# Kernel tuning notes

Measured on AMD Instinct MI355X. Metric: run time of the kernel, lower is better.

The kernel has to match this reference:

```python
import jax, jax.numpy as jnp
import numpy as np

B, N, G, D, H = 32, 512, 512, 512, 16
KD = D // H            # key_dim = embedding_dim // head_num
CLIP = 10.0            # tanh logit clipping


def _heads(x):
    # [B, C, D] -> [B, H, C, KD]
    b, c, _ = x.shape
    return x.reshape(b, c, H, KD).transpose(0, 2, 1, 3)


def setup_inputs() -> dict:
    key = jax.random.key(0)
    ks = jax.random.split(key, 9)
    s = 0.02
    return {
        "encoded_nodes": jax.random.normal(ks[0], (B, N, D), jnp.float32),
        "encoded_last": jax.random.normal(ks[1], (B, G, D), jnp.float32),
        "group_ninf_mask": jnp.zeros((B, G, N), jnp.float32),
        "Wq_graph": jax.random.normal(ks[2], (D, D), jnp.float32) * s,
        "Wq_first": jax.random.normal(ks[3], (D, D), jnp.float32) * s,
        "Wq_last": jax.random.normal(ks[4], (D, D), jnp.float32) * s,
        "Wk": jax.random.normal(ks[5], (D, D), jnp.float32) * s,
        "Wv": jax.random.normal(ks[6], (D, D), jnp.float32) * s,
        "Wcomb": jax.random.normal(ks[7], (D, D), jnp.float32) * s,
        "bcomb": jnp.zeros((D,), jnp.float32),
    }


def reference(encoded_nodes, encoded_last, group_ninf_mask,
              Wq_graph, Wq_first, Wq_last, Wk, Wv, Wcomb, bcomb):
    # reset(): graph embedding = mean over nodes, keys/values from encoded_nodes
    graph = encoded_nodes.mean(axis=1, keepdims=True)            # [B,1,D]
    q = (_heads(graph @ Wq_graph.T)                              # [B,H,1,KD] broadcast
         + _heads(encoded_last @ Wq_first.T)                     # q_first (first call)
         + _heads(encoded_last @ Wq_last.T))                     # [B,H,G,KD]
    k = _heads(encoded_nodes @ Wk.T)                             # [B,H,N,KD]
    v = _heads(encoded_nodes @ Wv.T)                             # [B,H,N,KD]

    # stage 1: masked multi-head attention
    score = jnp.einsum('bhgk,bhnk->bhgn', q, k) / float(np.sqrt(KD))
    score = score + group_ninf_mask[:, None, :, :]
    w = jax.nn.softmax(score, axis=-1)
    out = jnp.einsum('bhgn,bhnk->bhgk', w, v)
    out = out.transpose(0, 2, 1, 3).reshape(-1, G, D)            # [B,G,D]
    mh = out @ Wcomb.T + bcomb

    # stage 2: single-head score -> scale -> tanh clip -> mask -> softmax
    s2 = jnp.einsum('bgd,bnd->bgn', mh, encoded_nodes) / float(np.sqrt(D))
    s2 = CLIP * jnp.tanh(s2) + group_ninf_mask
    return jax.nn.softmax(s2, axis=-1)
```

## Files before the change

kernel.cpp:

```cpp
#include <hip/hip_runtime.h>
#include <hip/hip_bf16.h>
#include <stdint.h>
#include <math.h>

#define B_  32
#define N_  512
#define G_  512
#define D_  512
#define H_  16
#define KD_ 32

using bf16x8 = __attribute__((ext_vector_type(8))) short;
using f32x4  = __attribute__((ext_vector_type(4))) float;
typedef unsigned short u16;

__device__ __forceinline__ u16 f2b(float x) {
  union { __hip_bfloat16 h; u16 u; } c;
  c.h = __float2bfloat16(x);
  return c.u;
}
__device__ __forceinline__ float b2f(u16 u) {
  union { float f; unsigned int i; } c;
  c.i = ((unsigned int)u) << 16;
  return c.f;
}

__device__ __forceinline__ void async16(void* lds, const void* g) {
  __builtin_amdgcn_global_load_lds(
      (const __attribute__((address_space(1))) unsigned int*)(uintptr_t)g,
      (__attribute__((address_space(3))) unsigned int*)(uintptr_t)lds,
      16, 0, 0);
}

__global__ __launch_bounds__(512) void mean_split_kernel(
    const float* __restrict__ enc, u16* __restrict__ hi, u16* __restrict__ lo,
    float* __restrict__ partial)
{
  const int b  = blockIdx.x;
  const int nc = blockIdx.y;
  const int d  = threadIdx.x;
  const size_t base = ((size_t)b * N_ + (size_t)nc * 64) * D_ + d;
  float psum = 0.f;
  for (int i = 0; i < 64; ++i) {
    float v = enc[base + (size_t)i * D_];
    psum += v;
    u16 h = f2b(v);
    hi[base + (size_t)i * D_] = h;
    lo[base + (size_t)i * D_] = f2b(v - b2f(h));
  }
  partial[((size_t)b * 8 + nc) * D_ + d] = psum;
}

__global__ __launch_bounds__(512) void mean_final_kernel(
    const float* __restrict__ partial, float* __restrict__ graph)
{
  const int b = blockIdx.x, d = threadIdx.x;
  float s = 0.f;
  for (int c = 0; c < 8; ++c) s += partial[((size_t)b * 8 + c) * D_ + d];
  graph[b * D_ + d] = s * (1.0f / N_);
}

__global__ void split4_kernel(const float* __restrict__ in,
                              u16* __restrict__ hi, u16* __restrict__ lo, int n4)
{
  int i = blockIdx.x * blockDim.x + threadIdx.x;
  if (i < n4) {
    float4 v = ((const float4*)in)[i];
    ushort4 h, l;
    h.x = f2b(v.x); l.x = f2b(v.x - b2f(h.x));
    h.y = f2b(v.y); l.y = f2b(v.y - b2f(h.y));
    h.z = f2b(v.z); l.z = f2b(v.z - b2f(h.z));
    h.w = f2b(v.w); l.w = f2b(v.w - b2f(h.w));
    ((ushort4*)hi)[i] = h;
    ((ushort4*)lo)[i] = l;
  }
}

__global__ void wsum_split_kernel(const float* __restrict__ a, const float* __restrict__ b,
                                  u16* __restrict__ hi, u16* __restrict__ lo, int n4)
{
  int i = blockIdx.x * blockDim.x + threadIdx.x;
  if (i < n4) {
    float4 va = ((const float4*)a)[i];
    float4 vb = ((const float4*)b)[i];
    float x0 = va.x + vb.x, x1 = va.y + vb.y, x2 = va.z + vb.z, x3 = va.w + vb.w;
    ushort4 h, l;
    h.x = f2b(x0); l.x = f2b(x0 - b2f(h.x));
    h.y = f2b(x1); l.y = f2b(x1 - b2f(h.y));
    h.z = f2b(x2); l.z = f2b(x2 - b2f(h.z));
    h.w = f2b(x3); l.w = f2b(x3 - b2f(h.w));
    ((ushort4*)hi)[i] = h;
    ((ushort4*)lo)[i] = l;
  }
}

__global__ __launch_bounds__(256) void qg_kernel(
    const float* __restrict__ graph, const float* __restrict__ Wq,
    float* __restrict__ qg)
{
  const int b  = blockIdx.y;
  const int dd = blockIdx.x * 256 + threadIdx.x;
  const float* g = graph + b * D_;
  const float* w = Wq + (size_t)dd * D_;
  float s = 0.f;
  for (int k = 0; k < D_; ++k) s += g[k] * w[k];
  qg[b * D_ + dd] = s;
}

__global__ __launch_bounds__(256) void rowmax_kernel(
    const float* __restrict__ mask, float* __restrict__ rmx)
{
  const int row  = blockIdx.x * 4 + (threadIdx.x >> 6);
  const int lane = threadIdx.x & 63;
  const float* r = mask + (size_t)row * N_;
  float4 a  = *(const float4*)&r[lane * 8];
  float4 b4 = *(const float4*)&r[lane * 8 + 4];
  float m = fmaxf(fmaxf(fmaxf(a.x, a.y), fmaxf(a.z, a.w)),
                  fmaxf(fmaxf(b4.x, b4.y), fmaxf(b4.z, b4.w)));
#pragma unroll
  for (int w = 1; w < 64; w <<= 1) m = fmaxf(m, __shfl_xor(m, w));
  if (lane == 0) rmx[row] = m;
}

__global__ __launch_bounds__(64) void kmax_kernel(
    const u16* __restrict__ khi, float* __restrict__ kmx)
{
  const int b = blockIdx.x >> 4, h = blockIdx.x & 15;
  const int lane = threadIdx.x;
  float mx = 0.f;
  for (int i = 0; i < 8; ++i) {
    const int n = i * 64 + lane;
    const unsigned int* p =
        (const unsigned int*)&khi[((size_t)b * 512 + n) * 512 + h * 32];
    float s = 0.f;
#pragma unroll
    for (int w = 0; w < 16; ++w) {
      unsigned int u = p[w];
      float f0 = __uint_as_float(u << 16);
      float f1 = __uint_as_float(u & 0xffff0000u);
      s = fmaf(f0, f0, s);
      s = fmaf(f1, f1, s);
    }
    mx = fmaxf(mx, s);
  }
#pragma unroll
  for (int w = 1; w < 64; w <<= 1) mx = fmaxf(mx, __shfl_xor(mx, w));
  if (lane == 0) kmx[blockIdx.x] = sqrtf(mx) * 1.01f;
}

template<int OUTMODE, int BIASMODE>
__global__ __launch_bounds__(256) void gemm_split_kernel(
    const u16* __restrict__ Ahi, const u16* __restrict__ Alo,
    const u16* __restrict__ Bhi, const u16* __restrict__ Blo,
    void* __restrict__ Chi, void* __restrict__ Clo,
    void* __restrict__ Dhi, void* __restrict__ Dlo,
    const float* __restrict__ bias,
    int M, int N, int K)
{
  __shared__ __align__(16) u16 AhS[4096], AlS[4096], BhS[4096], BlS[4096];

  const int brow = blockIdx.y * 128;
  const int bcol = blockIdx.x * 128;
  const int tid  = threadIdx.x;
  const int wid  = tid >> 6;
  const int lane = tid & 63;
  const int wr = wid >> 1, wc = wid & 1;

  f32x4 acc[4][4] = {};

  const int c0   = wid * 2;
  const int srow = lane >> 2;
  const int skk  = (lane & 3) * 8;

  const size_t g0 = (size_t)(brow + c0 * 16      + srow) * K + skk;
  const size_t g1 = (size_t)(brow + c0 * 16 + 16 + srow) * K + skk;
  const size_t h0 = (size_t)(bcol + c0 * 16      + srow) * K + skk;
  const size_t h1 = (size_t)(bcol + c0 * 16 + 16 + srow) * K + skk;
  u16* lA0 = &AhS[c0 * 512]; u16* lA1 = &AhS[c0 * 512 + 512];
  u16* la0 = &AlS[c0 * 512]; u16* la1 = &AlS[c0 * 512 + 512];
  u16* lB0 = &BhS[c0 * 512]; u16* lB1 = &BhS[c0 * 512 + 512];
  u16* lb0 = &BlS[c0 * 512]; u16* lb1 = &BlS[c0 * 512 + 512];

  const int aoff = (wr * 64 + (lane & 15)) * 32 + (lane >> 4) * 8;
  const int boff = (wc * 64 + (lane & 15)) * 32 + (lane >> 4) * 8;

  for (int k0 = 0; k0 < K; k0 += 32) {
    async16(lA0, Ahi + g0 + k0);
    async16(lA1, Ahi + g1 + k0);
    async16(la0, Alo + g0 + k0);
    async16(la1, Alo + g1 + k0);
    async16(lB0, Bhi + h0 + k0);
    async16(lB1, Bhi + h1 + k0);
    async16(lb0, Blo + h0 + k0);
    async16(lb1, Blo + h1 + k0);
    __syncthreads();

    bf16x8 ah[4], al[4], bh[4], bl[4];
#pragma unroll
    for (int m = 0; m < 4; ++m) {
      ah[m] = *(const bf16x8*)&AhS[aoff + m * 512];
      al[m] = *(const bf16x8*)&AlS[aoff + m * 512];
    }
#pragma unroll
    for (int n = 0; n < 4; ++n) {
      bh[n] = *(const bf16x8*)&BhS[boff + n * 512];
      bl[n] = *(const bf16x8*)&BlS[boff + n * 512];
    }
#pragma unroll
    for (int m = 0; m < 4; ++m)
#pragma unroll
      for (int n = 0; n < 4; ++n) {
        f32x4 t = acc[m][n];
        t = __builtin_amdgcn_mfma_f32_16x16x32_bf16(al[m], bh[n], t, 0, 0, 0);
        t = __builtin_amdgcn_mfma_f32_16x16x32_bf16(ah[m], bl[n], t, 0, 0, 0);
        t = __builtin_amdgcn_mfma_f32_16x16x32_bf16(ah[m], bh[n], t, 0, 0, 0);
        acc[m][n] = t;
      }
    __syncthreads();
  }

  const int r0 = brow + wr * 64 + (lane >> 4) * 4;
  const int cbase = bcol + wc * 64 + (lane & 15);
#pragma unroll
  for (int m = 0; m < 4; ++m) {
#pragma unroll
    for (int n = 0; n < 4; ++n) {
      const int c = cbase + n * 16;
#pragma unroll
      for (int j = 0; j < 4; ++j) {
        const int r = r0 + m * 16 + j;
        float v = acc[m][n][j];
        if (BIASMODE == 1) v += bias[(r >> 9) * 512 + c];
        if (BIASMODE == 2) v += bias[c];
        u16 hv = f2b(v);
        u16 lv = f2b(v - b2f(hv));
        if (OUTMODE == 1) {
          ((u16*)Chi)[(size_t)r * N + c] = hv;
          ((u16*)Clo)[(size_t)r * N + c] = lv;
        } else {
          if (c < 512) {
            ((u16*)Chi)[(size_t)r * 512 + c] = hv;
            ((u16*)Clo)[(size_t)r * 512 + c] = lv;
          } else {
            const int bb = r >> 9, nn = r & 511, hh = (c >> 5) & 15, dd = c & 31;
            const size_t idx = (((size_t)bb * 16 + hh) * 32 + dd) * 512 + nn;
            ((u16*)Dhi)[idx] = hv;
            ((u16*)Dlo)[idx] = lv;
          }
        }
      }
    }
  }
}

__global__ __launch_bounds__(256) void attn_mfma5_kernel(
    u16* __restrict__ Qhi, u16* __restrict__ Qlo,
    const u16* __restrict__ Khi, const u16* __restrict__ Klo,
    const u16* __restrict__ VThi, const u16* __restrict__ VTlo,
    const float* __restrict__ mask,
    const float* __restrict__ rowmaxb,
    const float* __restrict__ kmaxb)
{
  __shared__ __align__(16) u16 Ph[4][32][56], Pl[4][32][56];

  const int tid = threadIdx.x, wid = tid >> 6, lane = tid & 63;
  const int id   = blockIdx.x;
  const int h    = id & 15;
  const int gblk = (id >> 4) & 3;
  const int b    = id >> 6;
  const int g0   = gblk * 128 + wid * 32;
  const int colq = lane & 15, rowg = lane >> 4;

  const size_t qb = ((size_t)b * G_ + g0) * D_ + h * KD_;
  const size_t kb = ((size_t)b * N_) * D_ + h * KD_;
  const size_t vb = (((size_t)b * H_ + h) * KD_) * (size_t)N_;
  const float* Mb = mask + ((size_t)b * G_ + g0) * N_;

  bf16x8 qh[2], ql[2];
  qh[0] = *(const bf16x8*)&Qhi[qb + (size_t)colq * D_ + rowg * 8];
  ql[0] = *(const bf16x8*)&Qlo[qb + (size_t)colq * D_ + rowg * 8];
  qh[1] = *(const bf16x8*)&Qhi[qb + (size_t)(16 + colq) * D_ + rowg * 8];
  ql[1] = *(const bf16x8*)&Qlo[qb + (size_t)(16 + colq) * D_ + rowg * 8];

  const float scale = 0.17677669529663687f;
  const f32x4 zf = {0.f, 0.f, 0.f, 0.f};
  const bf16x8 ones = {0x3F80, 0x3F80, 0x3F80, 0x3F80, 0x3F80, 0x3F80, 0x3F80, 0x3F80};

  const float km = kmaxb[b * 16 + h];
  float nq2[2];
#pragma unroll
  for (int rf = 0; rf < 2; ++rf) {
    float s = 0.f;
    const unsigned int* qw = (const unsigned int*)&qh[rf];
#pragma unroll
    for (int w = 0; w < 4; ++w) {
      unsigned int u = qw[w];
      float f0 = __uint_as_float(u << 16);
      float f1 = __uint_as_float(u & 0xffff0000u);
      s = fmaf(f0, f0, s);
      s = fmaf(f1, f1, s);
    }
    s += __shfl_xor(s, 16);
    s += __shfl_xor(s, 32);
    nq2[rf] = s;
  }
  float mrow[2][4];
#pragma unroll
  for (int rf = 0; rf < 2; ++rf)
#pragma unroll
    for (int j = 0; j < 4; ++j) {
      const int r16 = rowg * 4 + j;
      float nq = sqrtf(__shfl(nq2[rf], r16)) * 1.01f;
      mrow[rf][j] = scale * nq * km + rowmaxb[(size_t)b * G_ + g0 + rf * 16 + r16];
    }

  f32x4 o[2][2] = {};
  f32x4 os[2] = {};

  for (int n0 = 0; n0 < N_; n0 += 32) {
    bf16x8 kh0 = *(const bf16x8*)&Khi[kb + (size_t)(n0 + colq) * D_ + rowg * 8];
    bf16x8 kl0 = *(const bf16x8*)&Klo[kb + (size_t)(n0 + colq) * D_ + rowg * 8];
    bf16x8 kh1 = *(const bf16x8*)&Khi[kb + (size_t)(n0 + 16 + colq) * D_ + rowg * 8];
    bf16x8 kl1 = *(const bf16x8*)&Klo[kb + (size_t)(n0 + 16 + colq) * D_ + rowg * 8];
    bf16x8 vh0 = *(const bf16x8*)&VThi[vb + (size_t)colq * N_ + n0 + rowg * 8];
    bf16x8 vl0 = *(const bf16x8*)&VTlo[vb + (size_t)colq * N_ + n0 + rowg * 8];
    bf16x8 vh1 = *(const bf16x8*)&VThi[vb + (size_t)(16 + colq) * N_ + n0 + rowg * 8];
    bf16x8 vl1 = *(const bf16x8*)&VTlo[vb + (size_t)(16 + colq) * N_ + n0 + rowg * 8];

#pragma unroll
    for (int rf = 0; rf < 2; ++rf) {
      __builtin_amdgcn_s_setprio(1);
      f32x4 t0 = __builtin_amdgcn_mfma_f32_16x16x32_bf16(ql[rf], kh0, zf, 0, 0, 0);
      t0 = __builtin_amdgcn_mfma_f32_16x16x32_bf16(qh[rf], kl0, t0, 0, 0, 0);
      t0 = __builtin_amdgcn_mfma_f32_16x16x32_bf16(qh[rf], kh0, t0, 0, 0, 0);
      f32x4 t1 = __builtin_amdgcn_mfma_f32_16x16x32_bf16(ql[rf], kh1, zf, 0, 0, 0);
      t1 = __builtin_amdgcn_mfma_f32_16x16x32_bf16(qh[rf], kl1, t1, 0, 0, 0);
      t1 = __builtin_amdgcn_mfma_f32_16x16x32_bf16(qh[rf], kh1, t1, 0, 0, 0);
      __builtin_amdgcn_s_setprio(0);
#pragma unroll
      for (int j = 0; j < 4; ++j) {
        const int gg = rf * 16 + rowg * 4 + j;
        float m0 = Mb[(size_t)gg * N_ + n0 + colq];
        float m1 = Mb[(size_t)gg * N_ + n0 + 16 + colq];
        float p0 = __expf(fmaf(t0[j], scale, m0 - mrow[rf][j]));
        float p1 = __expf(fmaf(t1[j], scale, m1 - mrow[rf][j]));
        unsigned int uh, ul;
        asm("v_cvt_pk_bf16_f32 %0, %1, %2" : "=v"(uh) : "v"(p0), "v"(p1));
        float h0f = __uint_as_float(uh << 16);
        float h1f = __uint_as_float(uh & 0xffff0000u);
        float l0 = p0 - h0f, l1 = p1 - h1f;
        asm("v_cvt_pk_bf16_f32 %0, %1, %2" : "=v"(ul) : "v"(l0), "v"(l1));
        Ph[wid][gg][colq]      = (u16)uh;
        Ph[wid][gg][16 + colq] = (u16)(uh >> 16);
        Pl[wid][gg][colq]      = (u16)ul;
        Pl[wid][gg][16 + colq] = (u16)(ul >> 16);
      }
    }
    asm volatile("s_waitcnt lgkmcnt(0)" ::: "memory");

    bf16x8 ph0 = *(const bf16x8*)&Ph[wid][colq][rowg * 8];
    bf16x8 pl0 = *(const bf16x8*)&Pl[wid][colq][rowg * 8];
    bf16x8 ph1 = *(const bf16x8*)&Ph[wid][16 + colq][rowg * 8];
    bf16x8 pl1 = *(const bf16x8*)&Pl[wid][16 + colq][rowg * 8];

    __builtin_amdgcn_s_setprio(1);
    o[0][0] = __builtin_amdgcn_mfma_f32_16x16x32_bf16(pl0, vh0, o[0][0], 0, 0, 0);
    o[0][0] = __builtin_amdgcn_mfma_f32_16x16x32_bf16(ph0, vl0, o[0][0], 0, 0, 0);
    o[0][0] = __builtin_amdgcn_mfma_f32_16x16x32_bf16(ph0, vh0, o[0][0], 0, 0, 0);
    o[0][1] = __builtin_amdgcn_mfma_f32_16x16x32_bf16(pl0, vh1, o[0][1], 0, 0, 0);
    o[0][1] = __builtin_amdgcn_mfma_f32_16x16x32_bf16(ph0, vl1, o[0][1], 0, 0, 0);
    o[0][1] = __builtin_amdgcn_mfma_f32_16x16x32_bf16(ph0, vh1, o[0][1], 0, 0, 0);
    o[1][0] = __builtin_amdgcn_mfma_f32_16x16x32_bf16(pl1, vh0, o[1][0], 0, 0, 0);
    o[1][0] = __builtin_amdgcn_mfma_f32_16x16x32_bf16(ph1, vl0, o[1][0], 0, 0, 0);
    o[1][0] = __builtin_amdgcn_mfma_f32_16x16x32_bf16(ph1, vh0, o[1][0], 0, 0, 0);
    o[1][1] = __builtin_amdgcn_mfma_f32_16x16x32_bf16(pl1, vh1, o[1][1], 0, 0, 0);
    o[1][1] = __builtin_amdgcn_mfma_f32_16x16x32_bf16(ph1, vl1, o[1][1], 0, 0, 0);
    o[1][1] = __builtin_amdgcn_mfma_f32_16x16x32_bf16(ph1, vh1, o[1][1], 0, 0, 0);
    os[0] = __builtin_amdgcn_mfma_f32_16x16x32_bf16(ph0, ones, os[0], 0, 0, 0);
    os[0] = __builtin_amdgcn_mfma_f32_16x16x32_bf16(pl0, ones, os[0], 0, 0, 0);
    os[1] = __builtin_amdgcn_mfma_f32_16x16x32_bf16(ph1, ones, os[1], 0, 0, 0);
    os[1] = __builtin_amdgcn_mfma_f32_16x16x32_bf16(pl1, ones, os[1], 0, 0, 0);
    __builtin_amdgcn_s_setprio(0);
  }

#pragma unroll
  for (int rf = 0; rf < 2; ++rf)
#pragma unroll
    for (int j = 0; j < 4; ++j) {
      const float inv = 1.f / os[rf][j];
      const int gg = rf * 16 + rowg * 4 + j;
      float v0 = o[rf][0][j] * inv;
      float v1 = o[rf][1][j] * inv;
      u16 h0 = f2b(v0), h1 = f2b(v1);
      Qhi[qb + (size_t)gg * D_ + colq]      = h0;
      Qlo[qb + (size_t)gg * D_ + colq]      = f2b(v0 - b2f(h0));
      Qhi[qb + (size_t)gg * D_ + 16 + colq] = h1;
      Qlo[qb + (size_t)gg * D_ + 16 + colq] = f2b(v1 - b2f(h1));
    }
}

__global__ __launch_bounds__(256) void s2fused_kernel(
    const u16* __restrict__ Ahi, const u16* __restrict__ Alo,
    const u16* __restrict__ Bhi, const u16* __restrict__ Blo,
    const float* __restrict__ mask, float* __restrict__ out)
{
  __shared__ __align__(16) u16 AhS[2048], AlS[2048];
  __shared__ __align__(16) u16 BhS[16384], BlS[16384];

  const int z    = blockIdx.y;
  const int brow = blockIdx.x * 64;
  const int tid  = threadIdx.x;
  const int wid  = tid >> 6;
  const int lane = tid & 63;
  const int colq = lane & 15, rowg = lane >> 4;

  const u16* Az_hi = Ahi + (size_t)z * 262144;
  const u16* Az_lo = Alo + (size_t)z * 262144;
  const u16* Bz_hi = Bhi + (size_t)z * 262144;
  const u16* Bz_lo = Blo + (size_t)z * 262144;

  f32x4 acc[32] = {};

  const int srow = lane >> 2;
  const int skk  = (lane & 3) * 8;

  const size_t ga = (size_t)(brow + wid * 16 + srow) * 512 + skk;
  u16* lAh = &AhS[wid * 512];
  u16* lAl = &AlS[wid * 512];

  const int aoff = (wid * 16 + colq) * 32 + rowg * 8;

  for (int k0 = 0; k0 < 512; k0 += 32) {
    async16(lAh, Az_hi + ga + k0);
    async16(lAl, Az_lo + ga + k0);
#pragma unroll
    for (int c = 0; c < 8; ++c) {
      const int chunk = wid * 8 + c;
      const size_t gb = (size_t)(chunk * 16 + srow) * 512 + skk + k0;
      async16(&BhS[chunk * 512], Bz_hi + gb);
      async16(&BlS[chunk * 512], Bz_lo + gb);
    }
    __syncthreads();

    bf16x8 ah = *(const bf16x8*)&AhS[aoff];
    bf16x8 al = *(const bf16x8*)&AlS[aoff];
#pragma unroll
    for (int nf = 0; nf < 32; ++nf) {
      const int boff = (nf * 16 + colq) * 32 + rowg * 8;
      bf16x8 bh = *(const bf16x8*)&BhS[boff];
      bf16x8 bl = *(const bf16x8*)&BlS[boff];
      f32x4 t = acc[nf];
      t = __builtin_amdgcn_mfma_f32_16x16x32_bf16(al, bh, t, 0, 0, 0);
      t = __builtin_amdgcn_mfma_f32_16x16x32_bf16(ah, bl, t, 0, 0, 0);
      t = __builtin_amdgcn_mfma_f32_16x16x32_bf16(ah, bh, t, 0, 0, 0);
      acc[nf] = t;
    }
    __syncthreads();
  }

  const float iscale = 0.04419417382415922f;
  const size_t rbase = ((size_t)z * 512 + brow + wid * 16 + rowg * 4) * 512;

#pragma unroll
  for (int j = 0; j < 4; ++j) {
    const size_t roff = rbase + (size_t)j * 512 + colq;
#pragma unroll
    for (int nf = 0; nf < 32; ++nf) {
      float x  = acc[nf][j] * iscale;
      float e2 = __expf(2.f * x);
      float t  = 1.f - 2.f / (e2 + 1.f);
      acc[nf][j] = 10.f * t + mask[roff + nf * 16];
    }
  }
#pragma unroll
  for (int j = 0; j < 4; ++j) {
    float mx = acc[0][j];
#pragma unroll
    for (int nf = 1; nf < 32; ++nf) mx = fmaxf(mx, acc[nf][j]);
#pragma unroll
    for (int w = 1; w < 16; w <<= 1) mx = fmaxf(mx, __shfl_xor(mx, w));
    float sum = 0.f;
#pragma unroll
    for (int nf = 0; nf < 32; ++nf) {
      float e = __expf(acc[nf][j] - mx);
      acc[nf][j] = e;
      sum += e;
    }
#pragma unroll
    for (int w = 1; w < 16; w <<= 1) sum += __shfl_xor(sum, w);
    const float inv = 1.f / sum;
    const size_t roff = rbase + (size_t)j * 512 + colq;
#pragma unroll
    for (int nf = 0; nf < 32; ++nf)
      out[roff + nf * 16] = acc[nf][j] * inv;
  }
}

extern "C" void kernel_launch(void* const* d_in, const int* in_sizes, int n_in,
                              void* d_out, int out_size, void* d_ws, size_t ws_size,
                              hipStream_t stream)
{
  const float* enc_nodes = (const float*)d_in[0];
  const float* enc_last  = (const float*)d_in[1];
  const float* mask      = (const float*)d_in[2];
  const float* Wq_graph  = (const float*)d_in[3];
  const float* Wq_first  = (const float*)d_in[4];
  const float* Wq_last   = (const float*)d_in[5];
  const float* Wk        = (const float*)d_in[6];
  const float* Wv        = (const float*)d_in[7];
  const float* Wcomb     = (const float*)d_in[8];
  const float* bcomb     = (const float*)d_in[9];
  float* out = (float*)d_out;

  char* ws = (char*)d_ws;
  size_t off = 0;
  auto alloc = [&](size_t bytes) {
    void* p = ws + off;
    off += (bytes + 255) & ~(size_t)255;
    return p;
  };

  const size_t EL = (size_t)B_ * G_ * D_;
  u16* encNhi = (u16*)alloc(EL * 2);
  u16* encNlo = (u16*)alloc(EL * 2);
  u16* encLhi = (u16*)alloc(EL * 2);
  u16* encLlo = (u16*)alloc(EL * 2);
  u16* qhi    = (u16*)alloc(EL * 2);
  u16* qlo    = (u16*)alloc(EL * 2);
  u16* khi    = (u16*)alloc(EL * 2);
  u16* klo    = (u16*)alloc(EL * 2);
  u16* Wqlhi  = (u16*)alloc((size_t)D_ * D_ * 2);
  u16* Wqllo  = (u16*)alloc((size_t)D_ * D_ * 2);
  u16* Wkvhi  = (u16*)alloc((size_t)D_ * D_ * 4);
  u16* Wkvlo  = (u16*)alloc((size_t)D_ * D_ * 4);
  u16* Wchi   = (u16*)alloc((size_t)D_ * D_ * 2);
  u16* Wclo   = (u16*)alloc((size_t)D_ * D_ * 2);
  float* partial = (float*)alloc((size_t)B_ * 8 * D_ * 4);
  float* graph   = (float*)alloc((size_t)B_ * D_ * 4);
  float* qg      = (float*)alloc((size_t)B_ * D_ * 4);
  float* rowmaxb = (float*)alloc((size_t)B_ * G_ * 4);
  float* kmaxb   = (float*)alloc((size_t)B_ * H_ * 4);
  u16* vThi = encLhi; u16* vTlo = encLlo;
  u16* athi = qhi;    u16* atlo = qlo;
  u16* mhhi = khi;    u16* mhlo = klo;

  mean_split_kernel<<<dim3(32, 8), 512, 0, stream>>>(enc_nodes, encNhi, encNlo, partial);
  mean_final_kernel<<<dim3(32), 512, 0, stream>>>(partial, graph);
  split4_kernel<<<dim3(8192), 256, 0, stream>>>(enc_last, encLhi, encLlo, (int)(EL / 4));
  wsum_split_kernel<<<dim3(256), 256, 0, stream>>>(Wq_first, Wq_last, Wqlhi, Wqllo, 65536);
  split4_kernel<<<dim3(256), 256, 0, stream>>>(Wk, Wkvhi, Wkvlo, 65536);
  split4_kernel<<<dim3(256), 256, 0, stream>>>(Wv, Wkvhi + 262144, Wkvlo + 262144, 65536);
  split4_kernel<<<dim3(256), 256, 0, stream>>>(Wcomb, Wchi, Wclo, 65536);
  qg_kernel<<<dim3(2, 32), 256, 0, stream>>>(graph, Wq_graph, qg);
  rowmax_kernel<<<dim3(4096), 256, 0, stream>>>(mask, rowmaxb);

  gemm_split_kernel<1, 1><<<dim3(4, 128, 1), 256, 0, stream>>>(
      encLhi, encLlo, Wqlhi, Wqllo, qhi, qlo, nullptr, nullptr, qg,
      16384, 512, 512);
  gemm_split_kernel<3, 0><<<dim3(8, 128, 1), 256, 0, stream>>>(
      encNhi, encNlo, Wkvhi, Wkvlo, khi, klo, vThi, vTlo, nullptr,
      16384, 1024, 512);
  kmax_kernel<<<dim3(512), 64, 0, stream>>>(khi, kmaxb);

  attn_mfma5_kernel<<<dim3(2048), 256, 0, stream>>>(
      qhi, qlo, khi, klo, vThi, vTlo, mask, rowmaxb, kmaxb);

  gemm_split_kernel<1, 2><<<dim3(4, 128, 1), 256, 0, stream>>>(
      athi, atlo, Wchi, Wclo, mhhi, mhlo, nullptr, nullptr, bcomb,
      16384, 512, 512);

  s2fused_kernel<<<dim3(8, 32), 256, 0, stream>>>(
      mhhi, mhlo, encNhi, encNlo, mask, out);
}
```

Baseline: 508.8 us.

## Split stage-2 softmax columns across two waves and drop setprio in attention

The fused stage-2 score/softmax kernel now runs 512 threads per block. Each pair of waves splits the 512 output columns for one 16-row strip, which halves the per-wave accumulator count to lower register pressure and raise occupancy. The row max and sum are combined across the two waves through shared memory, at the cost of two extra block barriers. Separately, the s_setprio hints around the MFMA blocks in the attention kernel are removed.

```diff
diff --git a/kernel.cpp b/kernel.cpp
--- a/kernel.cpp
+++ b/kernel.cpp
@@ -253,7 +253,7 @@
   }
 }
 
-__global__ __launch_bounds__(256) void attn_mfma5_kernel(
+__global__ __launch_bounds__(256) void attn_mfma6_kernel(
     u16* __restrict__ Qhi, u16* __restrict__ Qlo,
     const u16* __restrict__ Khi, const u16* __restrict__ Klo,
     const u16* __restrict__ VThi, const u16* __restrict__ VTlo,
@@ -329,14 +329,12 @@
 
 #pragma unroll
     for (int rf = 0; rf < 2; ++rf) {
-      __builtin_amdgcn_s_setprio(1);
       f32x4 t0 = __builtin_amdgcn_mfma_f32_16x16x32_bf16(ql[rf], kh0, zf, 0, 0, 0);
       t0 = __builtin_amdgcn_mfma_f32_16x16x32_bf16(qh[rf], kl0, t0, 0, 0, 0);
       t0 = __builtin_amdgcn_mfma_f32_16x16x32_bf16(qh[rf], kh0, t0, 0, 0, 0);
       f32x4 t1 = __builtin_amdgcn_mfma_f32_16x16x32_bf16(ql[rf], kh1, zf, 0, 0, 0);
       t1 = __builtin_amdgcn_mfma_f32_16x16x32_bf16(qh[rf], kl1, t1, 0, 0, 0);
       t1 = __builtin_amdgcn_mfma_f32_16x16x32_bf16(qh[rf], kh1, t1, 0, 0, 0);
-      __builtin_amdgcn_s_setprio(0);
 #pragma unroll
       for (int j = 0; j < 4; ++j) {
         const int gg = rf * 16 + rowg * 4 + j;
@@ -363,7 +361,6 @@
     bf16x8 ph1 = *(const bf16x8*)&Ph[wid][16 + colq][rowg * 8];
     bf16x8 pl1 = *(const bf16x8*)&Pl[wid][16 + colq][rowg * 8];
 
-    __builtin_amdgcn_s_setprio(1);
     o[0][0] = __builtin_amdgcn_mfma_f32_16x16x32_bf16(pl0, vh0, o[0][0], 0, 0, 0);
     o[0][0] = __builtin_amdgcn_mfma_f32_16x16x32_bf16(ph0, vl0, o[0][0], 0, 0, 0);
     o[0][0] = __builtin_amdgcn_mfma_f32_16x16x32_bf16(ph0, vh0, o[0][0], 0, 0, 0);
@@ -380,7 +377,6 @@
     os[0] = __builtin_amdgcn_mfma_f32_16x16x32_bf16(pl0, ones, os[0], 0, 0, 0);
     os[1] = __builtin_amdgcn_mfma_f32_16x16x32_bf16(ph1, ones, os[1], 0, 0, 0);
     os[1] = __builtin_amdgcn_mfma_f32_16x16x32_bf16(pl1, ones, os[1], 0, 0, 0);
-    __builtin_amdgcn_s_setprio(0);
   }
 
 #pragma unroll
@@ -399,43 +395,46 @@
     }
 }
 
-__global__ __launch_bounds__(256) void s2fused_kernel(
+__global__ __launch_bounds__(512) void s2fused2_kernel(
     const u16* __restrict__ Ahi, const u16* __restrict__ Alo,
     const u16* __restrict__ Bhi, const u16* __restrict__ Blo,
     const float* __restrict__ mask, float* __restrict__ out)
 {
   __shared__ __align__(16) u16 AhS[2048], AlS[2048];
   __shared__ __align__(16) u16 BhS[16384], BlS[16384];
-
-  const int z    = blockIdx.y;
-  const int brow = blockIdx.x * 64;
+  __shared__ float Mx[4][16][2], Sm[4][16][2];
+
+  const int id   = blockIdx.x;
+  const int z    = id & 31;
+  const int brow = (id >> 5) * 64;
   const int tid  = threadIdx.x;
   const int wid  = tid >> 6;
   const int lane = tid & 63;
   const int colq = lane & 15, rowg = lane >> 4;
-
-  const u16* Az_hi = Ahi + (size_t)z * 262144;
-  const u16* Az_lo = Alo + (size_t)z * 262144;
-  const u16* Bz_hi = Bhi + (size_t)z * 262144;
-  const u16* Bz_lo = Blo + (size_t)z * 262144;
-
-  f32x4 acc[32] = {};
+  const int roww = wid >> 1, colw = wid & 1;
+
+  const size_t zoff = (size_t)z * 262144;
+  const u16* Az_hi = Ahi + zoff;
+  const u16* Az_lo = Alo + zoff;
+  const u16* Bz_hi = Bhi + zoff;
+  const u16* Bz_lo = Blo + zoff;
+
+  f32x4 acc[16] = {};
 
   const int srow = lane >> 2;
   const int skk  = (lane & 3) * 8;
 
   const size_t ga = (size_t)(brow + wid * 16 + srow) * 512 + skk;
-  u16* lAh = &AhS[wid * 512];
-  u16* lAl = &AlS[wid * 512];
-
-  const int aoff = (wid * 16 + colq) * 32 + rowg * 8;
+  const int aoff = (roww * 16 + colq) * 32 + rowg * 8;
 
   for (int k0 = 0; k0 < 512; k0 += 32) {
-    async16(lAh, Az_hi + ga + k0);
-    async16(lAl, Az_lo + ga + k0);
-#pragma unroll
-    for (int c = 0; c < 8; ++c) {
-      const int chunk = wid * 8 + c;
+    if (wid < 4) {
+      async16(&AhS[wid * 512], Az_hi + ga + k0);
+      async16(&AlS[wid * 512], Az_lo + ga + k0);
+    }
+#pragma unroll
+    for (int c = 0; c < 4; ++c) {
+      const int chunk = wid * 4 + c;
       const size_t gb = (size_t)(chunk * 16 + srow) * 512 + skk + k0;
       async16(&BhS[chunk * 512], Bz_hi + gb);
       async16(&BlS[chunk * 512], Bz_lo + gb);
@@ -445,8 +444,8 @@
     bf16x8 ah = *(const bf16x8*)&AhS[aoff];
     bf16x8 al = *(const bf16x8*)&AlS[aoff];
 #pragma unroll
-    for (int nf = 0; nf < 32; ++nf) {
-      const int boff = (nf * 16 + colq) * 32 + rowg * 8;
+    for (int nf = 0; nf < 16; ++nf) {
+      const int boff = (colw * 256 + nf * 16 + colq) * 32 + rowg * 8;
       bf16x8 bh = *(const bf16x8*)&BhS[boff];
       bf16x8 bl = *(const bf16x8*)&BlS[boff];
       f32x4 t = acc[nf];
@@ -459,39 +458,61 @@
   }
 
   const float iscale = 0.04419417382415922f;
-  const size_t rbase = ((size_t)z * 512 + brow + wid * 16 + rowg * 4) * 512;
+  const size_t rbase =
+      ((size_t)z * 512 + brow + roww * 16 + rowg * 4) * 512 + colw * 256 + colq;
 
 #pragma unroll
   for (int j = 0; j < 4; ++j) {
-    const size_t roff = rbase + (size_t)j * 512 + colq;
-#pragma unroll
-    for (int nf = 0; nf < 32; ++nf) {
+    const size_t roff = rbase + (size_t)j * 512;
+#pragma unroll
+    for (int nf = 0; nf < 16; ++nf) {
       float x  = acc[nf][j] * iscale;
       float e2 = __expf(2.f * x);
       float t  = 1.f - 2.f / (e2 + 1.f);
       acc[nf][j] = 10.f * t + mask[roff + nf * 16];
     }
   }
+  float mx4[4];
 #pragma unroll
   for (int j = 0; j < 4; ++j) {
     float mx = acc[0][j];
 #pragma unroll
-    for (int nf = 1; nf < 32; ++nf) mx = fmaxf(mx, acc[nf][j]);
+    for (int nf = 1; nf < 16; ++nf) mx = fmaxf(mx, acc[nf][j]);
 #pragma unroll
     for (int w = 1; w < 16; w <<= 1) mx = fmaxf(mx, __shfl_xor(mx, w));
+    mx4[j] = mx;
+  }
+  if (colq == 0) {
+#pragma unroll
+    for (int j = 0; j < 4; ++j) Mx[roww][rowg * 4 + j][colw] = mx4[j];
+  }
+  __syncthreads();
+  float sm4[4];
+#pragma unroll
+  for (int j = 0; j < 4; ++j) {
+    const float gmx = fmaxf(Mx[roww][rowg * 4 + j][0], Mx[roww][rowg * 4 + j][1]);
     float sum = 0.f;
 #pragma unroll
-    for (int nf = 0; nf < 32; ++nf) {
-      float e = __expf(acc[nf][j] - mx);
+    for (int nf = 0; nf < 16; ++nf) {
+      float e = __expf(acc[nf][j] - gmx);
       acc[nf][j] = e;
       sum += e;
     }
 #pragma unroll
     for (int w = 1; w < 16; w <<= 1) sum += __shfl_xor(sum, w);
-    const float inv = 1.f / sum;
-    const size_t roff = rbase + (size_t)j * 512 + colq;
-#pragma unroll
-    for (int nf = 0; nf < 32; ++nf)
+    sm4[j] = sum;
+  }
+  if (colq == 0) {
+#pragma unroll
+    for (int j = 0; j < 4; ++j) Sm[roww][rowg * 4 + j][colw] = sm4[j];
+  }
+  __syncthreads();
+#pragma unroll
+  for (int j = 0; j < 4; ++j) {
+    const float inv = 1.f / (Sm[roww][rowg * 4 + j][0] + Sm[roww][rowg * 4 + j][1]);
+    const size_t roff = rbase + (size_t)j * 512;
+#pragma unroll
+    for (int nf = 0; nf < 16; ++nf)
       out[roff + nf * 16] = acc[nf][j] * inv;
   }
 }
@@ -562,13 +583,13 @@
       16384, 1024, 512);
   kmax_kernel<<<dim3(512), 64, 0, stream>>>(khi, kmaxb);
 
-  attn_mfma5_kernel<<<dim3(2048), 256, 0, stream>>>(
+  attn_mfma6_kernel<<<dim3(2048), 256, 0, stream>>>(
       qhi, qlo, khi, klo, vThi, vTlo, mask, rowmaxb, kmaxb);
 
   gemm_split_kernel<1, 2><<<dim3(4, 128, 1), 256, 0, stream>>>(
       athi, atlo, Wchi, Wclo, mhhi, mhlo, nullptr, nullptr, bcomb,
       16384, 512, 512);
 
-  s2fused_kernel<<<dim3(8, 32), 256, 0, stream>>>(
+  s2fused2_kernel<<<dim3(256), 512, 0, stream>>>(
       mhhi, mhlo, encNhi, encNlo, mask, out);
 }
```

Measured after the change: 477.3 us. 6.2% less time.
